# Kernel optimization log

Measured on AMD Instinct MI355X. Metric: run time of the kernel, lower is better.

## Reference

```python
import jax, jax.numpy as jnp
import numpy as np

B, L, NE, DOUT = 4, 4096, 64, 64
DI = 128          # backbone model dim (hardcoded d_inner in MambaDoc)
NL = 2            # num_layers
H = 2             # num_heads
N = 128           # state_dim
G = 1             # num_groups
CONV = 4          # conv_size
DIN = 2 * DI      # expand=2 -> 256 inner channels of the mixer
P = DIN // H      # headdim = 128
CCH = DIN + 2 * G * N      # 512 conv channels (x, B, C)
DPROJ = 2 * DIN + 2 * G * N + H  # 770 in_proj output width


def setup_inputs() -> dict:
    key = jax.random.key(0)
    ks = jax.random.split(key, 8)
    s = lambda k, shape, sc: (jax.random.normal(k, shape, jnp.float32) * sc)
    return {
        "x": s(ks[0], (B, L, NE), 1.0),
        "in_w": s(ks[1], (DI, NE), (1.0 / NE) ** 0.5),
        "in_b": jnp.zeros((DI,), jnp.float32),
        "out_w": s(ks[2], (DOUT, DI), (1.0 / DI) ** 0.5),
        "out_b": jnp.zeros((DOUT,), jnp.float32),
        "l_rms_w": jnp.ones((NL, DI), jnp.float32),
        "l_in_w": s(ks[3], (NL, DPROJ, DI), (1.0 / DI) ** 0.5),
        "conv_w": s(ks[4], (NL, CCH, CONV), (1.0 / CONV) ** 0.5),
        "conv_b": jnp.zeros((NL, CCH), jnp.float32),
        "dt_bias": s(ks[5], (NL, H), 0.1),
        "A_log": jnp.zeros((NL, H), jnp.float32),   # A = -exp(A_log) = -1
        "D_p": jnp.ones((NL, H), jnp.float32),
        "gnorm_w": jnp.ones((NL, DIN), jnp.float32),
        "l_out_w": s(ks[6], (NL, DI, DIN), (1.0 / DIN) ** 0.5),
        "fnorm_w": jnp.ones((DI,), jnp.float32),
    }


def _rms(x, w, eps=1e-5):
    return x * jax.lax.rsqrt(jnp.mean(x * x, -1, keepdims=True) + eps) * w


def _mamba_layer(x, rms_w, in_w, cw, cb, dtb, a_log, d, gnw, ow):
    # x: (B,L,DI)
    h = _rms(x, rms_w)
    zxbcdt = jnp.einsum("bld,ed->ble", h, in_w)  # (B,L,770)
    z, xBC, dt = jnp.split(zxbcdt, [DIN, DIN + CCH], axis=-1)
    # causal depthwise conv over time, conv_size taps
    xp = jnp.pad(xBC, ((0, 0), (CONV - 1, 0), (0, 0)))
    xc = cb + sum(xp[:, k:k + L, :] * cw[:, k] for k in range(CONV))
    xc = jax.nn.silu(xc)
    xs, Bm, Cm = jnp.split(xc, [DIN, DIN + G * N], axis=-1)
    xs = xs.reshape(B, L, H, P)
    dt = jax.nn.softplus(dt + dtb)                 # (B,L,H)
    dA = jnp.exp(dt * (-jnp.exp(a_log)))           # (B,L,H) discrete decay

    def step(hc, inp):
        dA_t, dt_t, x_t, B_t, C_t = inp  # (B,H),(B,H),(B,H,P),(B,N),(B,N)
        hc = hc * dA_t[:, :, None, None] + (dt_t[:, :, None] * x_t)[..., None] * B_t[:, None, None, :]
        y = jnp.einsum("bhpn,bn->bhp", hc, C_t)
        return hc, y

    h0 = jnp.zeros((B, H, P, N), x.dtype)
    seq = (jnp.moveaxis(dA, 1, 0), jnp.moveaxis(dt, 1, 0), jnp.moveaxis(xs, 1, 0),
           jnp.moveaxis(Bm, 1, 0), jnp.moveaxis(Cm, 1, 0))
    _, ys = jax.lax.scan(step, h0, seq)
    y = jnp.moveaxis(ys, 0, 1)                     # (B,L,H,P)
    y = y + xs * d[None, None, :, None]            # D skip connection
    y = _rms(y.reshape(B, L, DIN) * jax.nn.silu(z), gnw)  # gated RMSNorm
    return x + jnp.einsum("ble,de->bld", y, ow)


def reference(x, in_w, in_b, out_w, out_b, l_rms_w, l_in_w, conv_w, conv_b,
              dt_bias, A_log, D_p, gnorm_w, l_out_w, fnorm_w):
    xp = jnp.einsum("bln,dn->bld", x, in_w) + in_b
    h = xp
    for i in range(NL):
        h = _mamba_layer(h, l_rms_w[i], l_in_w[i], conv_w[i], conv_b[i],
                         dt_bias[i], A_log[i], D_p[i], gnorm_w[i], l_out_w[i])
    h = _rms(h, fnorm_w)            # backbone final norm
    out = xp + h                    # outer residual in MambaDoc.forward
    return jnp.einsum("bld,od->blo", out, out_w) + out_b
```

## Files before the change

### kernel.cpp

```cpp
#include <hip/hip_runtime.h>
#include <cstddef>
#include <cstdint>


#define LSEQ 4096
#define MTOK 16384

typedef unsigned short u16;
typedef _Float16 f16x8 __attribute__((ext_vector_type(8)));
typedef float f32x4 __attribute__((ext_vector_type(4)));

__device__ __forceinline__ u16 f2h(float x) {
    return __builtin_bit_cast(u16, (_Float16)x);
}
__device__ __forceinline__ float h2f(u16 u) {
    return (float)__builtin_bit_cast(_Float16, u);
}
__device__ __forceinline__ float silu_f(float x) { return x / (1.f + __expf(-x)); }

__device__ __forceinline__ void async_lds16(const void* g, void* l) {
    __builtin_amdgcn_global_load_lds(
        (const __attribute__((address_space(1))) unsigned int*)g,
        (__attribute__((address_space(3))) unsigned int*)l, 16, 0, 0);
}

__device__ __forceinline__ uint4 cvt8(const float* __restrict__ src) {
    float4 a = *(const float4*)src;
    float4 b = *(const float4*)(src + 4);
    union { u16 u[8]; uint4 q; } pk;
    pk.u[0] = f2h(a.x); pk.u[1] = f2h(a.y); pk.u[2] = f2h(a.z); pk.u[3] = f2h(a.w);
    pk.u[4] = f2h(b.x); pk.u[5] = f2h(b.y); pk.u[6] = f2h(b.z); pk.u[7] = f2h(b.w);
    return pk.q;
}

__device__ __forceinline__ uint4 cvt8g(const float* __restrict__ src,
                                       const float* __restrict__ gw) {
    float4 a = *(const float4*)src;
    float4 b = *(const float4*)(src + 4);
    float4 ga = *(const float4*)gw;
    float4 gb = *(const float4*)(gw + 4);
    union { u16 u[8]; uint4 q; } pk;
    pk.u[0] = f2h(a.x * ga.x); pk.u[1] = f2h(a.y * ga.y);
    pk.u[2] = f2h(a.z * ga.z); pk.u[3] = f2h(a.w * ga.w);
    pk.u[4] = f2h(b.x * gb.x); pk.u[5] = f2h(b.y * gb.y);
    pk.u[6] = f2h(b.z * gb.z); pk.u[7] = f2h(b.w * gb.w);
    return pk.q;
}

__global__ __launch_bounds__(256) void gemm_rms0_kernel(
    const float* __restrict__ xf, const float* __restrict__ wf,
    const float* __restrict__ bias, const float* __restrict__ rmsw,
    u16* __restrict__ xp16, u16* __restrict__ hbuf16, u16* __restrict__ hn16)
{
    __shared__ u16 sA[64 * 64];
    __shared__ u16 sW[128 * 64];
    __shared__ float red[64][33];
    __shared__ float srstd[64];
    const int m0 = blockIdx.y * 64;
    const int tid = threadIdx.x, wid = tid >> 6, lane = tid & 63;
    const int wm = (wid >> 1) * 32, wn = (wid & 1) * 64;
    const int quad = lane >> 4, cl = lane & 15;
    #pragma unroll
    for (int i = 0; i < 2; i++) {
        int ck = i * 256 + tid;
        int r = ck >> 3, cc = ck & 7;
        int csw = (cc ^ (r & 7)) << 3;
        *(uint4*)&sA[ck * 8] = cvt8(xf + (size_t)(m0 + r) * 64 + csw);
    }
    #pragma unroll
    for (int i = 0; i < 4; i++) {
        int ck = i * 256 + tid;
        int r = ck >> 3, cc = ck & 7;
        int csw = (cc ^ (r & 7)) << 3;
        *(uint4*)&sW[ck * 8] = cvt8(wf + (size_t)r * 64 + csw);
    }
    __syncthreads();
    f32x4 acc[2][4];
    #pragma unroll
    for (int i = 0; i < 2; i++)
        #pragma unroll
        for (int j = 0; j < 4; j++) acc[i][j] = f32x4{0.f, 0.f, 0.f, 0.f};
    #pragma unroll
    for (int ks = 0; ks < 2; ks++) {
        f16x8 af[2], wv[4];
        int kc = ks * 4 + quad;
        #pragma unroll
        for (int i = 0; i < 2; i++) {
            int r = wm + i * 16 + cl;
            af[i] = *(const f16x8*)&sA[r * 64 + ((kc ^ (r & 7)) << 3)];
        }
        #pragma unroll
        for (int j = 0; j < 4; j++) {
            int r = wn + j * 16 + cl;
            wv[j] = *(const f16x8*)&sW[r * 64 + ((kc ^ (r & 7)) << 3)];
        }
        #pragma unroll
        for (int i = 0; i < 2; i++)
            #pragma unroll
            for (int j = 0; j < 4; j++)
                acc[i][j] = __builtin_amdgcn_mfma_f32_16x16x32_f16(
                    af[i], wv[j], acc[i][j], 0, 0, 0);
    }
    const int slot = (wid & 1) * 16 + cl;
    #pragma unroll
    for (int i = 0; i < 2; i++)
        #pragma unroll
        for (int r = 0; r < 4; r++) {
            int t = wm + i * 16 + quad * 4 + r;
            float ssp = 0.f;
            #pragma unroll
            for (int j = 0; j < 4; j++) {
                int n = wn + j * 16 + cl;
                float v = acc[i][j][r] + bias[n];
                acc[i][j][r] = v;
                ssp += v * v;
            }
            red[t][slot] = ssp;
        }
    __syncthreads();
    if (tid < 64) {
        float s = 0.f;
        #pragma unroll
        for (int sl = 0; sl < 32; sl++) s += red[tid][sl];
        srstd[tid] = rsqrtf(s * (1.f / 128.f) + 1e-5f);
    }
    __syncthreads();
    #pragma unroll
    for (int i = 0; i < 2; i++)
        #pragma unroll
        for (int r = 0; r < 4; r++) {
            int t = wm + i * 16 + quad * 4 + r;
            size_t ob = (size_t)(m0 + t) * 128;
            float rstd = srstd[t];
            #pragma unroll
            for (int j = 0; j < 4; j++) {
                int n = wn + j * 16 + cl;
                float v = acc[i][j][r];
                u16 vh = f2h(v);
                xp16[ob + n] = vh;
                hbuf16[ob + n] = vh;
                hn16[ob + n] = f2h(v * rstd * rmsw[n]);
            }
        }
}

__global__ __launch_bounds__(256) void gemm_inproj_kernel(
    const u16* __restrict__ A, const float* __restrict__ Wf,
    u16* __restrict__ zx16, float* __restrict__ dtb, float* __restrict__ Sb,
    const float* __restrict__ dt_bias, const float* __restrict__ A_log)
{
    __shared__ u16 sA[128 * 64];
    __shared__ u16 sW[128 * 64];
    __shared__ float sdt[2][128];
    const int K = 128, N = 770;
    const int n0 = blockIdx.x * 128, m0 = blockIdx.y * 128;
    const int tid = threadIdx.x, wid = tid >> 6, lane = tid & 63;
    const int wm = (wid >> 1) * 64, wn = (wid & 1) * 64;
    const int quad = lane >> 4, cl = lane & 15;
    f32x4 acc[4][4];
    #pragma unroll
    for (int i = 0; i < 4; i++)
        #pragma unroll
        for (int j = 0; j < 4; j++) acc[i][j] = f32x4{0.f, 0.f, 0.f, 0.f};

    for (int k0 = 0; k0 < K; k0 += 64) {
        #pragma unroll
        for (int i = 0; i < 4; i++) {
            int ck = i * 256 + tid;
            int r = ck >> 3, cc = ck & 7;
            int csw = (cc ^ (r & 7)) << 3;
            async_lds16(A + (size_t)(m0 + r) * K + k0 + csw,
                        (void*)(sA + (i * 256 + (tid & ~63)) * 8));
        }
        #pragma unroll
        for (int i = 0; i < 4; i++) {
            int ck = i * 256 + tid;
            int r = ck >> 3, cc = ck & 7;
            int csw = (cc ^ (r & 7)) << 3;
            int rr = n0 + r; if (rr >= N) rr = N - 1;
            *(uint4*)&sW[ck * 8] = cvt8(Wf + (size_t)rr * K + k0 + csw);
        }
        __syncthreads();
        #pragma unroll
        for (int ks = 0; ks < 2; ks++) {
            f16x8 af[4], wv[4];
            int kc = ks * 4 + quad;
            #pragma unroll
            for (int i = 0; i < 4; i++) {
                int r = wm + i * 16 + cl;
                af[i] = *(const f16x8*)&sA[r * 64 + ((kc ^ (r & 7)) << 3)];
            }
            #pragma unroll
            for (int j = 0; j < 4; j++) {
                int r = wn + j * 16 + cl;
                wv[j] = *(const f16x8*)&sW[r * 64 + ((kc ^ (r & 7)) << 3)];
            }
            #pragma unroll
            for (int i = 0; i < 4; i++)
                #pragma unroll
                for (int j = 0; j < 4; j++)
                    acc[i][j] = __builtin_amdgcn_mfma_f32_16x16x32_f16(
                        af[i], wv[j], acc[i][j], 0, 0, 0);
        }
        __syncthreads();
    }
    if (blockIdx.x < 6) {
        #pragma unroll
        for (int i = 0; i < 4; i++) {
            int m = m0 + wm + i * 16 + quad * 4;
            #pragma unroll
            for (int j = 0; j < 4; j++) {
                int n = n0 + wn + j * 16 + cl;
                #pragma unroll
                for (int r = 0; r < 4; r++)
                    zx16[(size_t)(m + r) * 768 + n] = f2h(acc[i][j][r]);
            }
        }
    } else {
        if ((wid & 1) == 0 && cl < 2) {
            #pragma unroll
            for (int i = 0; i < 4; i++)
                #pragma unroll
                for (int r = 0; r < 4; r++)
                    sdt[cl][wm + i * 16 + quad * 4 + r] = acc[i][0][r];
        }
        __syncthreads();
        const int hh = tid >> 7, t = tid & 127;
        float raw = sdt[hh][t] + dt_bias[hh];
        float dt = fmaxf(raw, 0.f) + log1pf(__expf(-fabsf(raw)));
        dtb[(size_t)(m0 + t) * 2 + hh] = dt;
        float ad = -__expf(A_log[hh]) * dt;
        __syncthreads();
        sdt[hh][t] = ad;
        __syncthreads();
        for (int off = 1; off < 128; off <<= 1) {
            float add = (t >= off) ? sdt[hh][t - off] : 0.f;
            __syncthreads();
            sdt[hh][t] += add;
            __syncthreads();
        }
        Sb[(size_t)(m0 + t) * 2 + hh] = sdt[hh][t];
    }
}

__global__ __launch_bounds__(512) void chunkstate_conv_kernel(
    const u16* __restrict__ zx16, const float* __restrict__ cw,
    const float* __restrict__ cb, const float* __restrict__ dtb,
    const float* __restrict__ Sb, u16* __restrict__ Hb)
{
    __shared__ u16 raw[2560 * 8];
    __shared__ u16 XT[128 * 128];
    __shared__ u16 BT[128 * 128];
    __shared__ float scw[2][128][4];
    __shared__ float scb[2][128];
    __shared__ float ssw[128];
    const int c = blockIdx.x, h = blockIdx.y, b = blockIdx.z;
    const int tid = threadIdx.x, wid = tid >> 6, lane = tid & 63;
    const int quad = lane >> 4, cl = lane & 15;
    const int tok0 = b * LSEQ + c * 128;
    for (int idx = tid; idx < 256; idx += 512) {
        int grp = idx >> 7, j = idx & 127;
        int ch = grp ? (256 + j) : (128 * h + j);
        float4 w4 = *(const float4*)&cw[ch * 4];
        scw[grp][j][0] = w4.x; scw[grp][j][1] = w4.y;
        scw[grp][j][2] = w4.z; scw[grp][j][3] = w4.w;
        scb[grp][j] = cb[ch];
    }
    if (tid < 128) {
        float Sl = Sb[(size_t)(tok0 + 127) * 2 + h];
        ssw[tid] = __expf(Sl - Sb[(size_t)(tok0 + tid) * 2 + h])
                   * dtb[(size_t)(tok0 + tid) * 2 + h];
    }
    #pragma unroll
    for (int i = 0; i < 5; i++) {
        int ck = i * 512 + tid;
        int r = ck >> 4; if (r > 130) r = 130;
        int cc = ck & 15;
        int tok = tok0 - 3 + r; if (tok < 0) tok = 0;
        async_lds16(zx16 + (size_t)tok * 768 + 256 + 128 * h + ((cc ^ (r & 15)) << 3),
                    (void*)(raw + (i * 512 + (tid & ~63)) * 8));
    }
    __syncthreads();
    if (c == 0 && tid < 48) *(uint4*)&raw[tid * 8] = make_uint4(0, 0, 0, 0);
    __syncthreads();
    #pragma unroll
    for (int it = 0; it < 4; it++) {
        int idx = it * 512 + tid;
        int s = idx & 127, pg = idx >> 7;
        f16x8 v[4];
        #pragma unroll
        for (int k = 0; k < 4; k++) {
            int rr = s + k;
            v[k] = *(const f16x8*)&raw[rr * 128 + ((pg ^ (rr & 15)) << 3)];
        }
        #pragma unroll
        for (int j = 0; j < 8; j++) {
            int p = pg * 8 + j;
            float o = scb[0][p] + (float)v[0][j] * scw[0][p][0]
                    + (float)v[1][j] * scw[0][p][1]
                    + (float)v[2][j] * scw[0][p][2]
                    + (float)v[3][j] * scw[0][p][3];
            o = silu_f(o);
            XT[p * 128 + (((s >> 3) ^ (p & 15)) << 3) + (s & 7)] = f2h(o);
        }
    }
    __syncthreads();
    #pragma unroll
    for (int i = 0; i < 5; i++) {
        int ck = i * 512 + tid;
        int r = ck >> 4; if (r > 130) r = 130;
        int cc = ck & 15;
        int tok = tok0 - 3 + r; if (tok < 0) tok = 0;
        async_lds16(zx16 + (size_t)tok * 768 + 512 + ((cc ^ (r & 15)) << 3),
                    (void*)(raw + (i * 512 + (tid & ~63)) * 8));
    }
    __syncthreads();
    if (c == 0 && tid < 48) *(uint4*)&raw[tid * 8] = make_uint4(0, 0, 0, 0);
    __syncthreads();
    #pragma unroll
    for (int it = 0; it < 4; it++) {
        int idx = it * 512 + tid;
        int s = idx & 127, ng = idx >> 7;
        f16x8 v[4];
        #pragma unroll
        for (int k = 0; k < 4; k++) {
            int rr = s + k;
            v[k] = *(const f16x8*)&raw[rr * 128 + ((ng ^ (rr & 15)) << 3)];
        }
        float wsv = ssw[s];
        #pragma unroll
        for (int j = 0; j < 8; j++) {
            int n = ng * 8 + j;
            float o = scb[1][n] + (float)v[0][j] * scw[1][n][0]
                    + (float)v[1][j] * scw[1][n][1]
                    + (float)v[2][j] * scw[1][n][2]
                    + (float)v[3][j] * scw[1][n][3];
            o = silu_f(o) * wsv;
            BT[n * 128 + (((s >> 3) ^ (n & 15)) << 3) + (s & 7)] = f2h(o);
        }
    }
    __syncthreads();
    const size_t blk = ((size_t)((b * 2 + h) * 32 + c)) << 14;
    const int wm = (wid >> 1) * 32, wn = (wid & 1) * 64;
    f32x4 acc[2][4];
    #pragma unroll
    for (int i = 0; i < 2; i++)
        #pragma unroll
        for (int j = 0; j < 4; j++) acc[i][j] = f32x4{0.f, 0.f, 0.f, 0.f};
    #pragma unroll
    for (int ks = 0; ks < 4; ks++) {
        f16x8 xa[2], bb[4];
        int kc = ks * 4 + quad;
        #pragma unroll
        for (int i = 0; i < 2; i++) {
            int r = wm + i * 16 + cl;
            xa[i] = *(const f16x8*)&XT[r * 128 + ((kc ^ (r & 15)) << 3)];
        }
        #pragma unroll
        for (int j = 0; j < 4; j++) {
            int r = wn + j * 16 + cl;
            bb[j] = *(const f16x8*)&BT[r * 128 + ((kc ^ (r & 15)) << 3)];
        }
        #pragma unroll
        for (int i = 0; i < 2; i++)
            #pragma unroll
            for (int j = 0; j < 4; j++)
                acc[i][j] = __builtin_amdgcn_mfma_f32_16x16x32_f16(
                    xa[i], bb[j], acc[i][j], 0, 0, 0);
    }
    u16* out = Hb + blk;
    #pragma unroll
    for (int i = 0; i < 2; i++)
        #pragma unroll
        for (int j = 0; j < 4; j++)
            #pragma unroll
            for (int r = 0; r < 4; r++)
                out[(size_t)(wm + i * 16 + quad * 4 + r) * 128 + wn + j * 16 + cl]
                    = f2h(acc[i][j][r]);
}

__global__ __launch_bounds__(256) void statecombine_kernel(
    const float* __restrict__ Sb, const u16* __restrict__ Hb,
    u16* __restrict__ Hbf)
{
    __shared__ float sdec[32];
    const int h = blockIdx.y, b = blockIdx.z;
    const int e2 = blockIdx.x * 256 + threadIdx.x;
    if (threadIdx.x < 32)
        sdec[threadIdx.x] =
            __expf(Sb[(size_t)(b * LSEQ + threadIdx.x * 128 + 127) * 2 + h]);
    const size_t base2 = ((size_t)((b * 2 + h) * 32)) << 13;
    const unsigned int* src = (const unsigned int*)Hb;
    unsigned int* dst = (unsigned int*)Hbf;
    unsigned int v[32];
    #pragma unroll
    for (int c = 0; c < 32; c++)
        v[c] = src[base2 + ((size_t)c << 13) + e2];
    __syncthreads();
    float s0 = 0.f, s1 = 0.f;
    #pragma unroll
    for (int c = 0; c < 32; c++) {
        union { u16 u[2]; unsigned int q; } pk;
        pk.u[0] = f2h(s0); pk.u[1] = f2h(s1);
        dst[base2 + ((size_t)c << 13) + e2] = pk.q;
        float d = sdec[c];
        s0 = d * s0 + h2f((u16)(v[c] & 0xffffu));
        s1 = d * s1 + h2f((u16)(v[c] >> 16));
    }
}

__global__ __launch_bounds__(512) void ssd_ph_kernel(
    const u16* __restrict__ zx16, const u16* __restrict__ Hbf,
    const float* __restrict__ dtb, const float* __restrict__ Sb,
    const float* __restrict__ cw, const float* __restrict__ cb,
    const float* __restrict__ Dp, u16* __restrict__ g16)
{
    __shared__ u16 raw[2560 * 8];
    __shared__ u16 XT[128 * 128];
    __shared__ u16 Btok[128 * 128];
    __shared__ u16 Ctok[128 * 128];
    __shared__ float sS[128], sdt[128];
    __shared__ float scw[3][128][4];
    __shared__ float scb[3][128];
    const int c = blockIdx.x, h = blockIdx.y, b = blockIdx.z;
    const int tid = threadIdx.x, wid = tid >> 6, lane = tid & 63;
    const int quad = lane >> 4, cl = lane & 15;
    const int tok0 = b * LSEQ + c * 128;
    const size_t blk = ((size_t)((b * 2 + h) * 32 + c)) << 14;
    for (int idx = tid; idx < 384; idx += 512) {
        int grp = idx >> 7, j = idx & 127;
        int ch = (grp == 0) ? (128 * h + j) : (grp == 1 ? 256 + j : 384 + j);
        float4 w4 = *(const float4*)&cw[ch * 4];
        scw[grp][j][0] = w4.x; scw[grp][j][1] = w4.y;
        scw[grp][j][2] = w4.z; scw[grp][j][3] = w4.w;
        scb[grp][j] = cb[ch];
    }
    if (tid < 128) {
        sS[tid] = Sb[(size_t)(tok0 + tid) * 2 + h];
        sdt[tid] = dtb[(size_t)(tok0 + tid) * 2 + h];
    }
    #pragma unroll
    for (int i = 0; i < 5; i++) {
        int ck = i * 512 + tid;
        int r = ck >> 4; if (r > 130) r = 130;
        int cc = ck & 15;
        int tok = tok0 - 3 + r; if (tok < 0) tok = 0;
        async_lds16(zx16 + (size_t)tok * 768 + 256 + 128 * h + ((cc ^ (r & 15)) << 3),
                    (void*)(raw + (i * 512 + (tid & ~63)) * 8));
    }
    __syncthreads();
    if (c == 0 && tid < 48) *(uint4*)&raw[tid * 8] = make_uint4(0, 0, 0, 0);
    __syncthreads();
    #pragma unroll
    for (int it = 0; it < 4; it++) {
        int idx = it * 512 + tid;
        int s = idx & 127, pg = idx >> 7;
        f16x8 v[4];
        #pragma unroll
        for (int k = 0; k < 4; k++) {
            int rr = s + k;
            v[k] = *(const f16x8*)&raw[rr * 128 + ((pg ^ (rr & 15)) << 3)];
        }
        #pragma unroll
        for (int j = 0; j < 8; j++) {
            int p = pg * 8 + j;
            float o = scb[0][p] + (float)v[0][j] * scw[0][p][0]
                    + (float)v[1][j] * scw[0][p][1]
                    + (float)v[2][j] * scw[0][p][2]
                    + (float)v[3][j] * scw[0][p][3];
            XT[p * 128 + (((s >> 3) ^ (p & 15)) << 3) + (s & 7)] = f2h(silu_f(o));
        }
    }
    __syncthreads();
    #pragma unroll
    for (int i = 0; i < 5; i++) {
        int ck = i * 512 + tid;
        int r = ck >> 4; if (r > 130) r = 130;
        int cc = ck & 15;
        int tok = tok0 - 3 + r; if (tok < 0) tok = 0;
        async_lds16(zx16 + (size_t)tok * 768 + 512 + ((cc ^ (r & 15)) << 3),
                    (void*)(raw + (i * 512 + (tid & ~63)) * 8));
    }
    __syncthreads();
    if (c == 0 && tid < 48) *(uint4*)&raw[tid * 8] = make_uint4(0, 0, 0, 0);
    __syncthreads();
    #pragma unroll
    for (int it = 0; it < 4; it++) {
        int idx = it * 512 + tid;
        int t = idx & 127, ng = idx >> 7;
        f16x8 v[4];
        #pragma unroll
        for (int k = 0; k < 4; k++) {
            int rr = t + k;
            v[k] = *(const f16x8*)&raw[rr * 128 + ((ng ^ (rr & 15)) << 3)];
        }
        union { u16 u[8]; uint4 q; } pk;
        #pragma unroll
        for (int j = 0; j < 8; j++) {
            int n = ng * 8 + j;
            float o = scb[1][n] + (float)v[0][j] * scw[1][n][0]
                    + (float)v[1][j] * scw[1][n][1]
                    + (float)v[2][j] * scw[1][n][2]
                    + (float)v[3][j] * scw[1][n][3];
            pk.u[j] = f2h(silu_f(o));
        }
        *(uint4*)&Btok[t * 128 + ((ng ^ (t & 15)) << 3)] = pk.q;
    }
    __syncthreads();
    #pragma unroll
    for (int i = 0; i < 5; i++) {
        int ck = i * 512 + tid;
        int r = ck >> 4; if (r > 130) r = 130;
        int cc = ck & 15;
        int tok = tok0 - 3 + r; if (tok < 0) tok = 0;
        async_lds16(zx16 + (size_t)tok * 768 + 640 + ((cc ^ (r & 15)) << 3),
                    (void*)(raw + (i * 512 + (tid & ~63)) * 8));
    }
    __syncthreads();
    if (c == 0 && tid < 48) *(uint4*)&raw[tid * 8] = make_uint4(0, 0, 0, 0);
    __syncthreads();
    #pragma unroll
    for (int it = 0; it < 4; it++) {
        int idx = it * 512 + tid;
        int t = idx & 127, ng = idx >> 7;
        f16x8 v[4];
        #pragma unroll
        for (int k = 0; k < 4; k++) {
            int rr = t + k;
            v[k] = *(const f16x8*)&raw[rr * 128 + ((ng ^ (rr & 15)) << 3)];
        }
        union { u16 u[8]; uint4 q; } pk;
        #pragma unroll
        for (int j = 0; j < 8; j++) {
            int n = ng * 8 + j;
            float o = scb[2][n] + (float)v[0][j] * scw[2][n][0]
                    + (float)v[1][j] * scw[2][n][1]
                    + (float)v[2][j] * scw[2][n][2]
                    + (float)v[3][j] * scw[2][n][3];
            pk.u[j] = f2h(silu_f(o));
        }
        *(uint4*)&Ctok[t * 128 + ((ng ^ (t & 15)) << 3)] = pk.q;
    }
    __syncthreads();
    #pragma unroll
    for (int i = 0; i < 4; i++) {
        int ck = i * 512 + tid;
        int r = ck >> 4, cc = ck & 15;
        async_lds16(Hbf + blk + (size_t)r * 128 + ((cc ^ (r & 15)) << 3),
                    (void*)(raw + (i * 512 + (tid & ~63)) * 8));
    }
    __syncthreads();
    const int wm = (wid >> 1) * 32, wn = (wid & 1) * 64;
    f32x4 acc[2][4];
    #pragma unroll
    for (int i = 0; i < 2; i++)
        #pragma unroll
        for (int j = 0; j < 4; j++) acc[i][j] = f32x4{0.f, 0.f, 0.f, 0.f};
    #pragma unroll
    for (int ks = 0; ks < 4; ks++) {
        f16x8 ca[2], hb[4];
        int kc = ks * 4 + quad;
        #pragma unroll
        for (int i = 0; i < 2; i++) {
            int r = wm + i * 16 + cl;
            ca[i] = *(const f16x8*)&Ctok[r * 128 + ((kc ^ (r & 15)) << 3)];
        }
        #pragma unroll
        for (int j = 0; j < 4; j++) {
            int r = wn + j * 16 + cl;
            hb[j] = *(const f16x8*)&raw[r * 128 + ((kc ^ (r & 15)) << 3)];
        }
        #pragma unroll
        for (int i = 0; i < 2; i++)
            #pragma unroll
            for (int j = 0; j < 4; j++)
                acc[i][j] = __builtin_amdgcn_mfma_f32_16x16x32_f16(
                    ca[i], hb[j], acc[i][j], 0, 0, 0);
    }
    #pragma unroll
    for (int i = 0; i < 2; i++)
        #pragma unroll
        for (int r = 0; r < 4; r++) {
            float e = __expf(sS[wm + i * 16 + quad * 4 + r]);
            #pragma unroll
            for (int j = 0; j < 4; j++) acc[i][j][r] *= e;
        }
    f32x4 sacc[2][4];
    #pragma unroll
    for (int i = 0; i < 2; i++)
        #pragma unroll
        for (int j = 0; j < 4; j++) sacc[i][j] = f32x4{0.f, 0.f, 0.f, 0.f};
    #pragma unroll
    for (int ks = 0; ks < 4; ks++) {
        f16x8 cs[2], bs[4];
        int kc = ks * 4 + quad;
        #pragma unroll
        for (int i2 = 0; i2 < 2; i2++) {
            int r = wm + i2 * 16 + cl;
            cs[i2] = *(const f16x8*)&Ctok[r * 128 + ((kc ^ (r & 15)) << 3)];
        }
        #pragma unroll
        for (int j = 0; j < 4; j++) {
            int r = wn + j * 16 + cl;
            bs[j] = *(const f16x8*)&Btok[r * 128 + ((kc ^ (r & 15)) << 3)];
        }
        #pragma unroll
        for (int i2 = 0; i2 < 2; i2++)
            #pragma unroll
            for (int j = 0; j < 4; j++)
                if (wm + i2 * 16 + 15 >= wn + j * 16)
                    sacc[i2][j] = __builtin_amdgcn_mfma_f32_16x16x32_f16(
                        cs[i2], bs[j], sacc[i2][j], 0, 0, 0);
    }
    __syncthreads();
    #pragma unroll
    for (int i2 = 0; i2 < 2; i2++)
        #pragma unroll
        for (int r = 0; r < 4; r++) {
            int t = wm + i2 * 16 + quad * 4 + r;
            float Stv = sS[t];
            #pragma unroll
            for (int j = 0; j < 4; j++) {
                int s = wn + j * 16 + cl;
                float gv = 0.f;
                if (s <= t) gv = sacc[i2][j][r] * __expf(Stv - sS[s]) * sdt[s];
                raw[t * 128 + (((s >> 3) ^ (t & 15)) << 3) + (s & 7)] = f2h(gv);
            }
        }
    __syncthreads();
    #pragma unroll
    for (int ks = 0; ks < 4; ks++) {
        f16x8 ga[2], xb[4];
        int kc = ks * 4 + quad;
        #pragma unroll
        for (int i = 0; i < 2; i++) {
            int r = wm + i * 16 + cl;
            ga[i] = *(const f16x8*)&raw[r * 128 + ((kc ^ (r & 15)) << 3)];
        }
        #pragma unroll
        for (int j = 0; j < 4; j++) {
            int r = wn + j * 16 + cl;
            xb[j] = *(const f16x8*)&XT[r * 128 + ((kc ^ (r & 15)) << 3)];
        }
        #pragma unroll
        for (int i = 0; i < 2; i++)
            #pragma unroll
            for (int j = 0; j < 4; j++)
                acc[i][j] = __builtin_amdgcn_mfma_f32_16x16x32_f16(
                    ga[i], xb[j], acc[i][j], 0, 0, 0);
    }
    const float dco = Dp[h];
    #pragma unroll
    for (int i = 0; i < 2; i++)
        #pragma unroll
        for (int r = 0; r < 4; r++) {
            int t = wm + i * 16 + quad * 4 + r;
            u16* row = g16 + (size_t)(tok0 + t) * 256 + h * 128;
            #pragma unroll
            for (int j = 0; j < 4; j++) {
                int p = wn + j * 16 + cl;
                float xv = h2f(XT[p * 128 + (((t >> 3) ^ (p & 15)) << 3) + (t & 7)]);
                float zv = h2f(zx16[(size_t)(tok0 + t) * 768 + h * 128 + p]);
                row[p] = f2h((acc[i][j][r] + dco * xv) * silu_f(zv));
            }
        }
}

__global__ __launch_bounds__(256) void gemm_outrms_kernel(
    const u16* __restrict__ A, const float* __restrict__ Wf,
    const float* __restrict__ gnw, const float* __restrict__ rmsw,
    u16* __restrict__ xp16, u16* __restrict__ hbuf16, u16* __restrict__ hn16,
    const float* __restrict__ out_wf, const float* __restrict__ out_b,
    float* __restrict__ dout, int mode)
{
    __shared__ u16 sA[64 * 64];
    __shared__ u16 sW[128 * 64];
    __shared__ float red[64][33];
    __shared__ float srstd[64];
    __shared__ float redp[64][5];
    __shared__ float rstdg[64];
    __shared__ u16 hn2[64 * 128];
    __shared__ u16 ow[64 * 128];
    const int K = 256;
    const int m0 = blockIdx.y * 64;
    const int tid = threadIdx.x, wid = tid >> 6, lane = tid & 63;
    const int wm = (wid >> 1) * 32, wn = (wid & 1) * 64;
    const int quad = lane >> 4, cl = lane & 15;
    f32x4 acc[2][4];
    #pragma unroll
    for (int i = 0; i < 2; i++)
        #pragma unroll
        for (int j = 0; j < 4; j++) acc[i][j] = f32x4{0.f, 0.f, 0.f, 0.f};

    float ssq = 0.f;
    for (int k0 = 0; k0 < K; k0 += 64) {
        #pragma unroll
        for (int i = 0; i < 2; i++) {
            int ck = i * 256 + tid;
            int r = ck >> 3, cc = ck & 7;
            int csw = (cc ^ (r & 7)) << 3;
            async_lds16(A + (size_t)(m0 + r) * K + k0 + csw,
                        (void*)(sA + (i * 256 + (tid & ~63)) * 8));
        }
        #pragma unroll
        for (int i = 0; i < 4; i++) {
            int ck = i * 256 + tid;
            int r = ck >> 3, cc = ck & 7;
            int csw = (cc ^ (r & 7)) << 3;
            *(uint4*)&sW[ck * 8] = cvt8g(Wf + (size_t)r * K + k0 + csw,
                                         gnw + k0 + csw);
        }
        __syncthreads();
        {
            int rr = tid >> 2, q = tid & 3;
            f16x8 v0 = *(const f16x8*)&sA[rr * 64 + q * 16];
            f16x8 v1 = *(const f16x8*)&sA[rr * 64 + q * 16 + 8];
            #pragma unroll
            for (int j = 0; j < 8; j++) {
                float a = (float)v0[j], bq = (float)v1[j];
                ssq += a * a + bq * bq;
            }
        }
        #pragma unroll
        for (int ks = 0; ks < 2; ks++) {
            f16x8 af[2], wv[4];
            int kc = ks * 4 + quad;
            #pragma unroll
            for (int i = 0; i < 2; i++) {
                int r = wm + i * 16 + cl;
                af[i] = *(const f16x8*)&sA[r * 64 + ((kc ^ (r & 7)) << 3)];
            }
            #pragma unroll
            for (int j = 0; j < 4; j++) {
                int r = wn + j * 16 + cl;
                wv[j] = *(const f16x8*)&sW[r * 64 + ((kc ^ (r & 7)) << 3)];
            }
            #pragma unroll
            for (int i = 0; i < 2; i++)
                #pragma unroll
                for (int j = 0; j < 4; j++)
                    acc[i][j] = __builtin_amdgcn_mfma_f32_16x16x32_f16(
                        af[i], wv[j], acc[i][j], 0, 0, 0);
        }
        __syncthreads();
    }
    redp[tid >> 2][tid & 3] = ssq;
    __syncthreads();
    if (tid < 64)
        rstdg[tid] = rsqrtf((redp[tid][0] + redp[tid][1] + redp[tid][2]
                             + redp[tid][3]) * (1.f / 256.f) + 1e-5f);
    __syncthreads();
    const int slot = (wid & 1) * 16 + cl;
    #pragma unroll
    for (int i = 0; i < 2; i++)
        #pragma unroll
        for (int r = 0; r < 4; r++) {
            int t = wm + i * 16 + quad * 4 + r;
            size_t ob = (size_t)(m0 + t) * 128;
            float rg = rstdg[t];
            float ssp = 0.f;
            #pragma unroll
            for (int j = 0; j < 4; j++) {
                int n = wn + j * 16 + cl;
                float v = acc[i][j][r] * rg + h2f(hbuf16[ob + n]);
                acc[i][j][r] = v;
                ssp += v * v;
            }
            red[t][slot] = ssp;
        }
    __syncthreads();
    if (tid < 64) {
        float s = 0.f;
        #pragma unroll
        for (int sl = 0; sl < 32; sl++) s += red[tid][sl];
        srstd[tid] = rsqrtf(s * (1.f / 128.f) + 1e-5f);
    }
    __syncthreads();
    #pragma unroll
    for (int i = 0; i < 2; i++)
        #pragma unroll
        for (int r = 0; r < 4; r++) {
            int t = wm + i * 16 + quad * 4 + r;
            size_t ob = (size_t)(m0 + t) * 128;
            float rstd = srstd[t];
            #pragma unroll
            for (int j = 0; j < 4; j++) {
                int n = wn + j * 16 + cl;
                float v = acc[i][j][r];
                float val = v * rstd * rmsw[n];
                if (mode == 1) {
                    hbuf16[ob + n] = f2h(v);
                    hn16[ob + n] = f2h(val);
                } else {
                    val += h2f(xp16[ob + n]);
                    hn2[t * 128 + (((n >> 3) ^ (t & 15)) << 3) + (n & 7)] = f2h(val);
                }
            }
        }
    if (mode == 1) return;
    #pragma unroll
    for (int i = 0; i < 4; i++) {
        int ck = i * 256 + tid;
        int rr = ck >> 4, cc = ck & 15;
        int csw = (cc ^ (rr & 15)) << 3;
        *(uint4*)&ow[ck * 8] = cvt8(out_wf + (size_t)rr * 128 + csw);
    }
    __syncthreads();
    const int wm4 = (wid >> 1) * 32, wn4 = (wid & 1) * 32;
    f32x4 acc2[2][2];
    #pragma unroll
    for (int i = 0; i < 2; i++)
        #pragma unroll
        for (int j = 0; j < 2; j++) acc2[i][j] = f32x4{0.f, 0.f, 0.f, 0.f};
    #pragma unroll
    for (int ks = 0; ks < 4; ks++) {
        f16x8 af2[2], wf2[2];
        int kc = ks * 4 + quad;
        #pragma unroll
        for (int i = 0; i < 2; i++) {
            int r = wm4 + i * 16 + cl;
            af2[i] = *(const f16x8*)&hn2[r * 128 + ((kc ^ (r & 15)) << 3)];
        }
        #pragma unroll
        for (int j = 0; j < 2; j++) {
            int rr = wn4 + j * 16 + cl;
            wf2[j] = *(const f16x8*)&ow[rr * 128 + ((kc ^ (rr & 15)) << 3)];
        }
        #pragma unroll
        for (int i = 0; i < 2; i++)
            #pragma unroll
            for (int j = 0; j < 2; j++)
                acc2[i][j] = __builtin_amdgcn_mfma_f32_16x16x32_f16(
                    af2[i], wf2[j], acc2[i][j], 0, 0, 0);
    }
    #pragma unroll
    for (int i = 0; i < 2; i++) {
        int m = m0 + wm4 + i * 16 + quad * 4;
        #pragma unroll
        for (int j = 0; j < 2; j++) {
            int n = wn4 + j * 16 + cl;
            float bv = out_b[n];
            #pragma unroll
            for (int r = 0; r < 4; r++)
                dout[(size_t)(m + r) * 64 + n] = acc2[i][j][r] + bv;
        }
    }
}

extern "C" void kernel_launch(void* const* d_in, const int* in_sizes, int n_in,
                              void* d_out, int out_size, void* d_ws, size_t ws_size,
                              hipStream_t stream)
{
    (void)in_sizes; (void)n_in; (void)out_size; (void)ws_size;
    const float* x       = (const float*)d_in[0];
    const float* in_w    = (const float*)d_in[1];
    const float* in_b    = (const float*)d_in[2];
    const float* out_w   = (const float*)d_in[3];
    const float* out_b   = (const float*)d_in[4];
    const float* l_rms_w = (const float*)d_in[5];
    const float* l_in_w  = (const float*)d_in[6];
    const float* conv_w  = (const float*)d_in[7];
    const float* conv_b  = (const float*)d_in[8];
    const float* dt_bias = (const float*)d_in[9];
    const float* A_log   = (const float*)d_in[10];
    const float* D_p     = (const float*)d_in[11];
    const float* gnorm_w = (const float*)d_in[12];
    const float* l_out_w = (const float*)d_in[13];
    const float* fnorm_w = (const float*)d_in[14];

    char* w = (char*)d_ws;
    u16*   xp16   = (u16*)(w);
    u16*   hbuf16 = (u16*)(w + 4194304);
    u16*   hn16   = (u16*)(w + 8388608);
    u16*   zx16   = (u16*)(w + 12582912);
    float* dtb    = (float*)(w + 37748736);
    float* Sb     = (float*)(w + 37879808);
    u16*   Hb     = (u16*)(w + 38010880);
    u16*   Hbf    = (u16*)(w + 46399488);
    u16*   g16    = (u16*)(w + 54788096);

    gemm_rms0_kernel<<<dim3(1, 256), 256, 0, stream>>>(
        x, in_w, in_b, l_rms_w, xp16, hbuf16, hn16);

    for (int i = 0; i < 2; i++) {
        gemm_inproj_kernel<<<dim3(7, 128), 256, 0, stream>>>(
            hn16, l_in_w + (size_t)i * 770 * 128, zx16, dtb, Sb,
            dt_bias + i * 2, A_log + i * 2);
        chunkstate_conv_kernel<<<dim3(32, 2, 4), 512, 0, stream>>>(
            zx16, conv_w + i * 2048, conv_b + i * 512, dtb, Sb, Hb);
        statecombine_kernel<<<dim3(32, 2, 4), 256, 0, stream>>>(Sb, Hb, Hbf);
        ssd_ph_kernel<<<dim3(32, 2, 4), 512, 0, stream>>>(
            zx16, Hbf, dtb, Sb, conv_w + i * 2048, conv_b + i * 512,
            D_p + i * 2, g16);
        gemm_outrms_kernel<<<dim3(1, 256), 256, 0, stream>>>(
            g16, l_out_w + (size_t)i * 128 * 256, gnorm_w + i * 256,
            (i == 0) ? (l_rms_w + 128) : fnorm_w, xp16, hbuf16, hn16,
            out_w, out_b, (float*)d_out, (i == 0) ? 1 : 3);
    }
}
```

Before: 226.1 us.

## Load conv windows directly into registers instead of staging through LDS

Both the chunk-state and SSD kernels now read the x/B/C conv input windows straight from global memory into registers. Each thread owns a group of 8 channels and 4 consecutive tokens and reuses 7 loaded rows across the 4 taps. This replaces the serialized async-LDS load, barrier and convert passes, and issues all loads up front, overlapped with the Hbf async load in the SSD kernel. It removes several barriers and shrinks LDS use, which may raise occupancy. The cost is higher register pressure and redundant global reads of overlapping rows.

```diff
diff --git a/kernel.cpp b/kernel.cpp
--- a/kernel.cpp
+++ b/kernel.cpp
@@ -248,7 +248,6 @@
     const float* __restrict__ cb, const float* __restrict__ dtb,
     const float* __restrict__ Sb, u16* __restrict__ Hb)
 {
-    __shared__ u16 raw[2560 * 8];
     __shared__ u16 XT[128 * 128];
     __shared__ u16 BT[128 * 128];
     __shared__ float scw[2][128][4];
@@ -271,70 +270,54 @@
         ssw[tid] = __expf(Sl - Sb[(size_t)(tok0 + tid) * 2 + h])
                    * dtb[(size_t)(tok0 + tid) * 2 + h];
     }
-    #pragma unroll
-    for (int i = 0; i < 5; i++) {
-        int ck = i * 512 + tid;
-        int r = ck >> 4; if (r > 130) r = 130;
-        int cc = ck & 15;
-        int tok = tok0 - 3 + r; if (tok < 0) tok = 0;
-        async_lds16(zx16 + (size_t)tok * 768 + 256 + 128 * h + ((cc ^ (r & 15)) << 3),
-                    (void*)(raw + (i * 512 + (tid & ~63)) * 8));
-    }
-    __syncthreads();
-    if (c == 0 && tid < 48) *(uint4*)&raw[tid * 8] = make_uint4(0, 0, 0, 0);
-    __syncthreads();
-    #pragma unroll
-    for (int it = 0; it < 4; it++) {
-        int idx = it * 512 + tid;
-        int s = idx & 127, pg = idx >> 7;
-        f16x8 v[4];
-        #pragma unroll
-        for (int k = 0; k < 4; k++) {
-            int rr = s + k;
-            v[k] = *(const f16x8*)&raw[rr * 128 + ((pg ^ (rr & 15)) << 3)];
-        }
-        #pragma unroll
-        for (int j = 0; j < 8; j++) {
-            int p = pg * 8 + j;
-            float o = scb[0][p] + (float)v[0][j] * scw[0][p][0]
-                    + (float)v[1][j] * scw[0][p][1]
-                    + (float)v[2][j] * scw[0][p][2]
-                    + (float)v[3][j] * scw[0][p][3];
-            o = silu_f(o);
-            XT[p * 128 + (((s >> 3) ^ (p & 15)) << 3) + (s & 7)] = f2h(o);
-        }
-    }
-    __syncthreads();
-    #pragma unroll
-    for (int i = 0; i < 5; i++) {
-        int ck = i * 512 + tid;
-        int r = ck >> 4; if (r > 130) r = 130;
-        int cc = ck & 15;
-        int tok = tok0 - 3 + r; if (tok < 0) tok = 0;
-        async_lds16(zx16 + (size_t)tok * 768 + 512 + ((cc ^ (r & 15)) << 3),
-                    (void*)(raw + (i * 512 + (tid & ~63)) * 8));
-    }
-    __syncthreads();
-    if (c == 0 && tid < 48) *(uint4*)&raw[tid * 8] = make_uint4(0, 0, 0, 0);
-    __syncthreads();
-    #pragma unroll
-    for (int it = 0; it < 4; it++) {
-        int idx = it * 512 + tid;
-        int s = idx & 127, ng = idx >> 7;
-        f16x8 v[4];
-        #pragma unroll
-        for (int k = 0; k < 4; k++) {
-            int rr = s + k;
-            v[k] = *(const f16x8*)&raw[rr * 128 + ((ng ^ (rr & 15)) << 3)];
-        }
+    const int pg = tid >> 5, sb = tid & 31, s0 = sb * 4;
+    const u16* gx = zx16 + 256 + 128 * h + pg * 8;
+    const u16* gb = zx16 + 512 + pg * 8;
+    uint4 vX[7], vB[7];
+    #pragma unroll
+    for (int i = 0; i < 7; i++) {
+        int q = s0 - 3 + i;
+        bool zer = (c == 0) && (q < 0);
+        int qq = zer ? 0 : q;
+        size_t off = (size_t)(tok0 + qq) * 768;
+        uint4 xv = *(const uint4*)(gx + off);
+        uint4 bv = *(const uint4*)(gb + off);
+        vX[i] = zer ? make_uint4(0u, 0u, 0u, 0u) : xv;
+        vB[i] = zer ? make_uint4(0u, 0u, 0u, 0u) : bv;
+    }
+    __syncthreads();
+    #pragma unroll
+    for (int j = 0; j < 4; j++) {
+        int s = s0 + j;
+        f16x8 a0 = __builtin_bit_cast(f16x8, vX[j]);
+        f16x8 a1 = __builtin_bit_cast(f16x8, vX[j + 1]);
+        f16x8 a2 = __builtin_bit_cast(f16x8, vX[j + 2]);
+        f16x8 a3 = __builtin_bit_cast(f16x8, vX[j + 3]);
+        #pragma unroll
+        for (int jj = 0; jj < 8; jj++) {
+            int p = pg * 8 + jj;
+            float o = scb[0][p] + (float)a0[jj] * scw[0][p][0]
+                    + (float)a1[jj] * scw[0][p][1]
+                    + (float)a2[jj] * scw[0][p][2]
+                    + (float)a3[jj] * scw[0][p][3];
+            XT[p * 128 + (((s >> 3) ^ (p & 15)) << 3) + (s & 7)] = f2h(silu_f(o));
+        }
+    }
+    #pragma unroll
+    for (int j = 0; j < 4; j++) {
+        int s = s0 + j;
         float wsv = ssw[s];
-        #pragma unroll
-        for (int j = 0; j < 8; j++) {
-            int n = ng * 8 + j;
-            float o = scb[1][n] + (float)v[0][j] * scw[1][n][0]
-                    + (float)v[1][j] * scw[1][n][1]
-                    + (float)v[2][j] * scw[1][n][2]
-                    + (float)v[3][j] * scw[1][n][3];
+        f16x8 a0 = __builtin_bit_cast(f16x8, vB[j]);
+        f16x8 a1 = __builtin_bit_cast(f16x8, vB[j + 1]);
+        f16x8 a2 = __builtin_bit_cast(f16x8, vB[j + 2]);
+        f16x8 a3 = __builtin_bit_cast(f16x8, vB[j + 3]);
+        #pragma unroll
+        for (int jj = 0; jj < 8; jj++) {
+            int n = pg * 8 + jj;
+            float o = scb[1][n] + (float)a0[jj] * scw[1][n][0]
+                    + (float)a1[jj] * scw[1][n][1]
+                    + (float)a2[jj] * scw[1][n][2]
+                    + (float)a3[jj] * scw[1][n][3];
             o = silu_f(o) * wsv;
             BT[n * 128 + (((s >> 3) ^ (n & 15)) << 3) + (s & 7)] = f2h(o);
         }
@@ -415,7 +398,7 @@
     const float* __restrict__ cw, const float* __restrict__ cb,
     const float* __restrict__ Dp, u16* __restrict__ g16)
 {
-    __shared__ u16 raw[2560 * 8];
+    __shared__ u16 raw[128 * 128];
     __shared__ u16 XT[128 * 128];
     __shared__ u16 Btok[128 * 128];
     __shared__ u16 Ctok[128 * 128];
@@ -440,114 +423,85 @@
         sdt[tid] = dtb[(size_t)(tok0 + tid) * 2 + h];
     }
     #pragma unroll
-    for (int i = 0; i < 5; i++) {
-        int ck = i * 512 + tid;
-        int r = ck >> 4; if (r > 130) r = 130;
-        int cc = ck & 15;
-        int tok = tok0 - 3 + r; if (tok < 0) tok = 0;
-        async_lds16(zx16 + (size_t)tok * 768 + 256 + 128 * h + ((cc ^ (r & 15)) << 3),
-                    (void*)(raw + (i * 512 + (tid & ~63)) * 8));
-    }
-    __syncthreads();
-    if (c == 0 && tid < 48) *(uint4*)&raw[tid * 8] = make_uint4(0, 0, 0, 0);
-    __syncthreads();
-    #pragma unroll
-    for (int it = 0; it < 4; it++) {
-        int idx = it * 512 + tid;
-        int s = idx & 127, pg = idx >> 7;
-        f16x8 v[4];
-        #pragma unroll
-        for (int k = 0; k < 4; k++) {
-            int rr = s + k;
-            v[k] = *(const f16x8*)&raw[rr * 128 + ((pg ^ (rr & 15)) << 3)];
-        }
-        #pragma unroll
-        for (int j = 0; j < 8; j++) {
-            int p = pg * 8 + j;
-            float o = scb[0][p] + (float)v[0][j] * scw[0][p][0]
-                    + (float)v[1][j] * scw[0][p][1]
-                    + (float)v[2][j] * scw[0][p][2]
-                    + (float)v[3][j] * scw[0][p][3];
-            XT[p * 128 + (((s >> 3) ^ (p & 15)) << 3) + (s & 7)] = f2h(silu_f(o));
-        }
-    }
-    __syncthreads();
-    #pragma unroll
-    for (int i = 0; i < 5; i++) {
-        int ck = i * 512 + tid;
-        int r = ck >> 4; if (r > 130) r = 130;
-        int cc = ck & 15;
-        int tok = tok0 - 3 + r; if (tok < 0) tok = 0;
-        async_lds16(zx16 + (size_t)tok * 768 + 512 + ((cc ^ (r & 15)) << 3),
-                    (void*)(raw + (i * 512 + (tid & ~63)) * 8));
-    }
-    __syncthreads();
-    if (c == 0 && tid < 48) *(uint4*)&raw[tid * 8] = make_uint4(0, 0, 0, 0);
-    __syncthreads();
-    #pragma unroll
-    for (int it = 0; it < 4; it++) {
-        int idx = it * 512 + tid;
-        int t = idx & 127, ng = idx >> 7;
-        f16x8 v[4];
-        #pragma unroll
-        for (int k = 0; k < 4; k++) {
-            int rr = t + k;
-            v[k] = *(const f16x8*)&raw[rr * 128 + ((ng ^ (rr & 15)) << 3)];
-        }
-        union { u16 u[8]; uint4 q; } pk;
-        #pragma unroll
-        for (int j = 0; j < 8; j++) {
-            int n = ng * 8 + j;
-            float o = scb[1][n] + (float)v[0][j] * scw[1][n][0]
-                    + (float)v[1][j] * scw[1][n][1]
-                    + (float)v[2][j] * scw[1][n][2]
-                    + (float)v[3][j] * scw[1][n][3];
-            pk.u[j] = f2h(silu_f(o));
-        }
-        *(uint4*)&Btok[t * 128 + ((ng ^ (t & 15)) << 3)] = pk.q;
-    }
-    __syncthreads();
-    #pragma unroll
-    for (int i = 0; i < 5; i++) {
-        int ck = i * 512 + tid;
-        int r = ck >> 4; if (r > 130) r = 130;
-        int cc = ck & 15;
-        int tok = tok0 - 3 + r; if (tok < 0) tok = 0;
-        async_lds16(zx16 + (size_t)tok * 768 + 640 + ((cc ^ (r & 15)) << 3),
-                    (void*)(raw + (i * 512 + (tid & ~63)) * 8));
-    }
-    __syncthreads();
-    if (c == 0 && tid < 48) *(uint4*)&raw[tid * 8] = make_uint4(0, 0, 0, 0);
-    __syncthreads();
-    #pragma unroll
-    for (int it = 0; it < 4; it++) {
-        int idx = it * 512 + tid;
-        int t = idx & 127, ng = idx >> 7;
-        f16x8 v[4];
-        #pragma unroll
-        for (int k = 0; k < 4; k++) {
-            int rr = t + k;
-            v[k] = *(const f16x8*)&raw[rr * 128 + ((ng ^ (rr & 15)) << 3)];
-        }
-        union { u16 u[8]; uint4 q; } pk;
-        #pragma unroll
-        for (int j = 0; j < 8; j++) {
-            int n = ng * 8 + j;
-            float o = scb[2][n] + (float)v[0][j] * scw[2][n][0]
-                    + (float)v[1][j] * scw[2][n][1]
-                    + (float)v[2][j] * scw[2][n][2]
-                    + (float)v[3][j] * scw[2][n][3];
-            pk.u[j] = f2h(silu_f(o));
-        }
-        *(uint4*)&Ctok[t * 128 + ((ng ^ (t & 15)) << 3)] = pk.q;
-    }
-    __syncthreads();
-    #pragma unroll
     for (int i = 0; i < 4; i++) {
         int ck = i * 512 + tid;
         int r = ck >> 4, cc = ck & 15;
         async_lds16(Hbf + blk + (size_t)r * 128 + ((cc ^ (r & 15)) << 3),
                     (void*)(raw + (i * 512 + (tid & ~63)) * 8));
+    }
+    const int pg = tid >> 5, sb = tid & 31, s0 = sb * 4;
+    const u16* gx = zx16 + 256 + 128 * h + pg * 8;
+    const u16* gb = zx16 + 512 + pg * 8;
+    const u16* gc = zx16 + 640 + pg * 8;
+    uint4 vX[7], vB[7], vC[7];
+    #pragma unroll
+    for (int i = 0; i < 7; i++) {
+        int q = s0 - 3 + i;
+        bool zer = (c == 0) && (q < 0);
+        int qq = zer ? 0 : q;
+        size_t off = (size_t)(tok0 + qq) * 768;
+        uint4 xv = *(const uint4*)(gx + off);
+        uint4 bv = *(const uint4*)(gb + off);
+        uint4 cv = *(const uint4*)(gc + off);
+        vX[i] = zer ? make_uint4(0u, 0u, 0u, 0u) : xv;
+        vB[i] = zer ? make_uint4(0u, 0u, 0u, 0u) : bv;
+        vC[i] = zer ? make_uint4(0u, 0u, 0u, 0u) : cv;
+    }
+    __syncthreads();
+    #pragma unroll
+    for (int j = 0; j < 4; j++) {
+        int s = s0 + j;
+        f16x8 a0 = __builtin_bit_cast(f16x8, vX[j]);
+        f16x8 a1 = __builtin_bit_cast(f16x8, vX[j + 1]);
+        f16x8 a2 = __builtin_bit_cast(f16x8, vX[j + 2]);
+        f16x8 a3 = __builtin_bit_cast(f16x8, vX[j + 3]);
+        #pragma unroll
+        for (int jj = 0; jj < 8; jj++) {
+            int p = pg * 8 + jj;
+            float o = scb[0][p] + (float)a0[jj] * scw[0][p][0]
+                    + (float)a1[jj] * scw[0][p][1]
+                    + (float)a2[jj] * scw[0][p][2]
+                    + (float)a3[jj] * scw[0][p][3];
+            XT[p * 128 + (((s >> 3) ^ (p & 15)) << 3) + (s & 7)] = f2h(silu_f(o));
+        }
+    }
+    #pragma unroll
+    for (int j = 0; j < 4; j++) {
+        int t = s0 + j;
+        f16x8 a0 = __builtin_bit_cast(f16x8, vB[j]);
+        f16x8 a1 = __builtin_bit_cast(f16x8, vB[j + 1]);
+        f16x8 a2 = __builtin_bit_cast(f16x8, vB[j + 2]);
+        f16x8 a3 = __builtin_bit_cast(f16x8, vB[j + 3]);
+        union { u16 u[8]; uint4 q; } pk;
+        #pragma unroll
+        for (int jj = 0; jj < 8; jj++) {
+            int n = pg * 8 + jj;
+            float o = scb[1][n] + (float)a0[jj] * scw[1][n][0]
+                    + (float)a1[jj] * scw[1][n][1]
+                    + (float)a2[jj] * scw[1][n][2]
+                    + (float)a3[jj] * scw[1][n][3];
+            pk.u[jj] = f2h(silu_f(o));
+        }
+        *(uint4*)&Btok[t * 128 + ((pg ^ (t & 15)) << 3)] = pk.q;
+    }
+    #pragma unroll
+    for (int j = 0; j < 4; j++) {
+        int t = s0 + j;
+        f16x8 a0 = __builtin_bit_cast(f16x8, vC[j]);
+        f16x8 a1 = __builtin_bit_cast(f16x8, vC[j + 1]);
+        f16x8 a2 = __builtin_bit_cast(f16x8, vC[j + 2]);
+        f16x8 a3 = __builtin_bit_cast(f16x8, vC[j + 3]);
+        union { u16 u[8]; uint4 q; } pk;
+        #pragma unroll
+        for (int jj = 0; jj < 8; jj++) {
+            int n = pg * 8 + jj;
+            float o = scb[2][n] + (float)a0[jj] * scw[2][n][0]
+                    + (float)a1[jj] * scw[2][n][1]
+                    + (float)a2[jj] * scw[2][n][2]
+                    + (float)a3[jj] * scw[2][n][3];
+            pk.u[jj] = f2h(silu_f(o));
+        }
+        *(uint4*)&Ctok[t * 128 + ((pg ^ (t & 15)) << 3)] = pk.q;
     }
     __syncthreads();
     const int wm = (wid >> 1) * 32, wn = (wid & 1) * 64;
```

Result: no change. 229.6 us (+1.6%).
